# Kernel tuning notes

Measured on AMD Instinct MI355X. Metric: run time of the kernel, lower is better.

The kernel has to match this reference:

```python
import jax, jax.numpy as jnp
import numpy as np

L2_REG = 0.02


def setup_inputs() -> dict:
    key = jax.random.key(0)
    k1, k2 = jax.random.split(key)
    n, d = 4096, 1024
    anchors = jax.random.normal(k1, (n, d), dtype=jnp.float32)
    positives = jax.random.normal(k2, (n, d), dtype=jnp.float32)
    return {"anchors": anchors, "positives": positives}


def reference(anchors, positives):
    # Fused equivalent of the per-row masked_select loop:
    # x[i, j] = a_i . (p_j - p_i) = S[i, j] - S[i, i], for j != i
    n = anchors.shape[0]
    S = anchors @ positives.T                     # (n, n)
    x = S - jnp.diag(S)[:, None]                  # subtract anchor-positive sim per row
    offdiag = ~jnp.eye(n, dtype=bool)
    # sum over negatives j != i of exp(x[i, j])
    s = jnp.sum(jnp.where(offdiag, jnp.exp(x), 0.0), axis=1)  # (n,)
    n_pair = jnp.mean(jnp.log1p(s))
    l2 = jnp.sum(anchors ** 2 + positives ** 2) / n
    return n_pair + L2_REG * l2
```

## Files before the change

### kernel.cpp

```cpp
#include <hip/hip_runtime.h>
#include <math.h>
#include <stdint.h>

#define N 4096
#define Dm 1024
#define BM 128
#define BN 128
#define BK 32
#define NCB (N / 64)

typedef __attribute__((ext_vector_type(8))) short bf16x8;
typedef __attribute__((ext_vector_type(4))) float f32x4;

typedef const void __attribute__((address_space(1)))* gas_t;
typedef void __attribute__((address_space(3)))* las_t;

static __device__ __forceinline__ void gload_lds16(const void* g, void* l) {
    __builtin_amdgcn_global_load_lds((gas_t)g, (las_t)l, 16, 0, 0);
}

static __device__ __forceinline__ unsigned short f2bf(float f) {
    unsigned int u = __float_as_uint(f);
    unsigned int r = (u + 0x7fff + ((u >> 16) & 1)) >> 16;
    return (unsigned short)r;
}

__global__ __launch_bounds__(256) void prep_kernel(const float* __restrict__ A,
                                                   const float* __restrict__ P,
                                                   unsigned short* __restrict__ Abf,
                                                   unsigned short* __restrict__ Pbf,
                                                   float* __restrict__ D,
                                                   float* __restrict__ rowl2) {
    int row = blockIdx.x;
    int t = threadIdx.x;
    const float4* a4 = (const float4*)(A + (size_t)row * Dm);
    const float4* p4 = (const float4*)(P + (size_t)row * Dm);
    float4 a = a4[t], p = p4[t];
    ushort4 ab, pb;
    ab.x = f2bf(a.x); ab.y = f2bf(a.y); ab.z = f2bf(a.z); ab.w = f2bf(a.w);
    pb.x = f2bf(p.x); pb.y = f2bf(p.y); pb.z = f2bf(p.z); pb.w = f2bf(p.w);
    ((ushort4*)(Abf + (size_t)row * Dm))[t] = ab;
    ((ushort4*)(Pbf + (size_t)row * Dm))[t] = pb;
    float dot = a.x * p.x + a.y * p.y + a.z * p.z + a.w * p.w;
    float l2  = a.x * a.x + a.y * a.y + a.z * a.z + a.w * a.w
              + p.x * p.x + p.y * p.y + p.z * p.z + p.w * p.w;
#pragma unroll
    for (int off = 32; off; off >>= 1) {
        dot += __shfl_xor(dot, off, 64);
        l2  += __shfl_xor(l2,  off, 64);
    }
    __shared__ float sd[4], sl[4];
    int wave = t >> 6;
    if ((t & 63) == 0) { sd[wave] = dot; sl[wave] = l2; }
    __syncthreads();
    if (t == 0) {
        D[row]     = sd[0] + sd[1] + sd[2] + sd[3];
        rowl2[row] = sl[0] + sl[1] + sl[2] + sl[3];
    }
}

__global__ __launch_bounds__(256) void npair_mfma(const unsigned short* __restrict__ Abf,
                                                  const unsigned short* __restrict__ Pbf,
                                                  const float* __restrict__ D,
                                                  float* __restrict__ Mpart,
                                                  float* __restrict__ Spart) {
    __shared__ unsigned short At[BM * BK];
    __shared__ unsigned short Bt[BN * BK];
    int tid = threadIdx.x;
    int wid = tid >> 6, lane = tid & 63;
    int wr = wid >> 1, wc = wid & 1;
    int row0 = blockIdx.y * BM, col0 = blockIdx.x * BN;

    int r0 = tid >> 2,        kq0 = (tid & 3) << 3;
    int r1 = (256 + tid) >> 2, kq1 = (tid & 3) << 3;
    const unsigned short* Ag0 = Abf + (size_t)(row0 + r0) * Dm + kq0;
    const unsigned short* Ag1 = Abf + (size_t)(row0 + r1) * Dm + kq1;
    const unsigned short* Bg0 = Pbf + (size_t)(col0 + r0) * Dm + kq0;
    const unsigned short* Bg1 = Pbf + (size_t)(col0 + r1) * Dm + kq1;
    unsigned short* Al0 = At + (size_t)tid * 8;
    unsigned short* Al1 = At + (size_t)(256 + tid) * 8;
    unsigned short* Bl0 = Bt + (size_t)tid * 8;
    unsigned short* Bl1 = Bt + (size_t)(256 + tid) * 8;

    f32x4 acc[4][4] = {};

    for (int kt = 0; kt < Dm; kt += BK) {
        __syncthreads();
        gload_lds16(Ag0 + kt, Al0);
        gload_lds16(Ag1 + kt, Al1);
        gload_lds16(Bg0 + kt, Bl0);
        gload_lds16(Bg1 + kt, Bl1);
        __syncthreads();

        bf16x8 af[4], bfr[4];
#pragma unroll
        for (int i = 0; i < 4; ++i) {
            int arow = wr * 64 + i * 16 + (lane & 15);
            af[i]  = *(const bf16x8*)(At + arow * BK + ((lane >> 4) << 3));
            int brow = wc * 64 + i * 16 + (lane & 15);
            bfr[i] = *(const bf16x8*)(Bt + brow * BK + ((lane >> 4) << 3));
        }
#pragma unroll
        for (int i = 0; i < 4; ++i)
#pragma unroll
            for (int j = 0; j < 4; ++j)
                acc[i][j] = __builtin_amdgcn_mfma_f32_16x16x32_bf16(af[i], bfr[j], acc[i][j], 0, 0, 0);
    }

    int cb = blockIdx.x * 2 + wc;
#pragma unroll
    for (int rt = 0; rt < 4; ++rt) {
        int rbase = row0 + wr * 64 + rt * 16 + ((lane >> 4) << 2);
#pragma unroll
        for (int e = 0; e < 4; ++e) {
            int gr = rbase + e;
            float Dv = D[gr];
            float xs[4];
            float m = -INFINITY;
#pragma unroll
            for (int ct = 0; ct < 4; ++ct) {
                int gc = col0 + wc * 64 + ct * 16 + (lane & 15);
                float x = acc[rt][ct][e] - Dv;
                if (gr == gc) x = -INFINITY;
                xs[ct] = x;
                m = fmaxf(m, x);
            }
#pragma unroll
            for (int off = 8; off; off >>= 1) m = fmaxf(m, __shfl_xor(m, off, 64));
            float s = 0.0f;
#pragma unroll
            for (int ct = 0; ct < 4; ++ct) s += __expf(xs[ct] - m);
#pragma unroll
            for (int off = 8; off; off >>= 1) s += __shfl_xor(s, off, 64);
            if ((lane & 15) == 0) {
                Mpart[(size_t)gr * NCB + cb] = m;
                Spart[(size_t)gr * NCB + cb] = s;
            }
        }
    }
}

__global__ __launch_bounds__(256) void combine_rows(const float* __restrict__ Mpart,
                                                    const float* __restrict__ Spart,
                                                    float* __restrict__ loss) {
    int t = threadIdx.x;
    int lane = t & 63;
    int row = blockIdx.x * 4 + (t >> 6);
    float mp = Mpart[(size_t)row * NCB + lane];
    float sp = Spart[(size_t)row * NCB + lane];
    float m = mp;
#pragma unroll
    for (int off = 32; off; off >>= 1) m = fmaxf(m, __shfl_xor(m, off, 64));
    float s = sp * __expf(mp - m);
#pragma unroll
    for (int off = 32; off; off >>= 1) s += __shfl_xor(s, off, 64);
    if (lane == 0) loss[row] = m + logf(__expf(-m) + s);
}

__global__ __launch_bounds__(256) void final_reduce(const float* __restrict__ loss,
                                                    const float* __restrict__ rowl2,
                                                    float* __restrict__ out) {
    int t = threadIdx.x;
    float accL = 0.0f, acc2 = 0.0f;
    for (int i = t; i < N; i += 256) {
        accL += loss[i];
        acc2 += rowl2[i];
    }
#pragma unroll
    for (int off = 32; off; off >>= 1) {
        accL += __shfl_xor(accL, off, 64);
        acc2 += __shfl_xor(acc2, off, 64);
    }
    __shared__ float sa[4], sb[4];
    int wave = t >> 6;
    if ((t & 63) == 0) { sa[wave] = accL; sb[wave] = acc2; }
    __syncthreads();
    if (t == 0) {
        float L  = sa[0] + sa[1] + sa[2] + sa[3];
        float l2 = sb[0] + sb[1] + sb[2] + sb[3];
        out[0] = L / (float)N + 0.02f * (l2 / (float)N);
    }
}

extern "C" void kernel_launch(void* const* d_in, const int* in_sizes, int n_in,
                              void* d_out, int out_size, void* d_ws, size_t ws_size,
                              hipStream_t stream) {
    const float* A = (const float*)d_in[0];
    const float* P = (const float*)d_in[1];
    float* out = (float*)d_out;

    unsigned short* Abf = (unsigned short*)d_ws;
    unsigned short* Pbf = Abf + (size_t)N * Dm;
    float* D     = (float*)(Pbf + (size_t)N * Dm);
    float* rowl2 = D + N;
    float* loss  = rowl2 + N;
    float* Mpart = loss + N;
    float* Spart = Mpart + (size_t)N * NCB;

    prep_kernel<<<N, 256, 0, stream>>>(A, P, Abf, Pbf, D, rowl2);
    dim3 grid(N / BN, N / BM);
    npair_mfma<<<grid, 256, 0, stream>>>(Abf, Pbf, D, Mpart, Spart);
    combine_rows<<<N / 4, 256, 0, stream>>>(Mpart, Spart, loss);
    final_reduce<<<1, 256, 0, stream>>>(loss, rowl2, out);
}
```

Measured before the change: 141.6 us.

## Double K tile to 64 with XOR-swizzled LDS layout and cache D in shared memory

Raises the K tile from 32 to 64, so the main loop runs half as many iterations and the load/barrier overhead per MFMA is halved. The global-to-LDS copy now places 16-byte chunks under an XOR swizzle keyed on row, and the fragment reads apply the same swizzle to avoid LDS bank conflicts. The diagonal values D for the block's rows are staged in shared memory for the epilogue. LDS use doubles to 32KB, which may lower occupancy.

Result: faster. 132.1 us (-6.7%).

```diff
diff --git a/kernel.cpp b/kernel.cpp
--- a/kernel.cpp
+++ b/kernel.cpp
@@ -6,7 +6,7 @@
 #define Dm 1024
 #define BM 128
 #define BN 128
-#define BK 32
+#define BK 64
 #define NCB (N / 64)
 
 typedef __attribute__((ext_vector_type(8))) short bf16x8;
@@ -66,55 +66,63 @@
                                                   float* __restrict__ Spart) {
     __shared__ unsigned short At[BM * BK];
     __shared__ unsigned short Bt[BN * BK];
+    __shared__ float Ds[BM];
     int tid = threadIdx.x;
     int wid = tid >> 6, lane = tid & 63;
     int wr = wid >> 1, wc = wid & 1;
     int row0 = blockIdx.y * BM, col0 = blockIdx.x * BN;
 
-    int r0 = tid >> 2,        kq0 = (tid & 3) << 3;
-    int r1 = (256 + tid) >> 2, kq1 = (tid & 3) << 3;
-    const unsigned short* Ag0 = Abf + (size_t)(row0 + r0) * Dm + kq0;
-    const unsigned short* Ag1 = Abf + (size_t)(row0 + r1) * Dm + kq1;
-    const unsigned short* Bg0 = Pbf + (size_t)(col0 + r0) * Dm + kq0;
-    const unsigned short* Bg1 = Pbf + (size_t)(col0 + r1) * Dm + kq1;
-    unsigned short* Al0 = At + (size_t)tid * 8;
-    unsigned short* Al1 = At + (size_t)(256 + tid) * 8;
-    unsigned short* Bl0 = Bt + (size_t)tid * 8;
-    unsigned short* Bl1 = Bt + (size_t)(256 + tid) * 8;
+    const unsigned short* gA[4]; const unsigned short* gB[4];
+    unsigned short* lA[4]; unsigned short* lB[4];
+#pragma unroll
+    for (int b = 0; b < 4; ++b) {
+        int L = b * 256 + tid;
+        int row = L >> 3, c = L & 7;
+        int kch = c ^ (row & 7);
+        gA[b] = Abf + (size_t)(row0 + row) * Dm + (kch << 3);
+        gB[b] = Pbf + (size_t)(col0 + row) * Dm + (kch << 3);
+        lA[b] = At + (size_t)L * 8;
+        lB[b] = Bt + (size_t)L * 8;
+    }
+    if (tid < BM) Ds[tid] = D[row0 + tid];
 
     f32x4 acc[4][4] = {};
 
     for (int kt = 0; kt < Dm; kt += BK) {
         __syncthreads();
-        gload_lds16(Ag0 + kt, Al0);
-        gload_lds16(Ag1 + kt, Al1);
-        gload_lds16(Bg0 + kt, Bl0);
-        gload_lds16(Bg1 + kt, Bl1);
+#pragma unroll
+        for (int b = 0; b < 4; ++b) {
+            gload_lds16(gA[b] + kt, lA[b]);
+            gload_lds16(gB[b] + kt, lB[b]);
+        }
         __syncthreads();
-
-        bf16x8 af[4], bfr[4];
-#pragma unroll
-        for (int i = 0; i < 4; ++i) {
-            int arow = wr * 64 + i * 16 + (lane & 15);
-            af[i]  = *(const bf16x8*)(At + arow * BK + ((lane >> 4) << 3));
-            int brow = wc * 64 + i * 16 + (lane & 15);
-            bfr[i] = *(const bf16x8*)(Bt + brow * BK + ((lane >> 4) << 3));
+#pragma unroll
+        for (int ks = 0; ks < 2; ++ks) {
+            bf16x8 af[4], bfr[4];
+#pragma unroll
+            for (int i = 0; i < 4; ++i) {
+                int g = (ks << 2) + (lane >> 4);
+                int arow = wr * 64 + i * 16 + (lane & 15);
+                af[i]  = *(const bf16x8*)(At + arow * BK + ((g ^ (arow & 7)) << 3));
+                int brow = wc * 64 + i * 16 + (lane & 15);
+                bfr[i] = *(const bf16x8*)(Bt + brow * BK + ((g ^ (brow & 7)) << 3));
+            }
+#pragma unroll
+            for (int i = 0; i < 4; ++i)
+#pragma unroll
+                for (int j = 0; j < 4; ++j)
+                    acc[i][j] = __builtin_amdgcn_mfma_f32_16x16x32_bf16(af[i], bfr[j], acc[i][j], 0, 0, 0);
         }
-#pragma unroll
-        for (int i = 0; i < 4; ++i)
-#pragma unroll
-            for (int j = 0; j < 4; ++j)
-                acc[i][j] = __builtin_amdgcn_mfma_f32_16x16x32_bf16(af[i], bfr[j], acc[i][j], 0, 0, 0);
     }
 
     int cb = blockIdx.x * 2 + wc;
 #pragma unroll
     for (int rt = 0; rt < 4; ++rt) {
-        int rbase = row0 + wr * 64 + rt * 16 + ((lane >> 4) << 2);
+        int rloc = wr * 64 + rt * 16 + ((lane >> 4) << 2);
 #pragma unroll
         for (int e = 0; e < 4; ++e) {
-            int gr = rbase + e;
-            float Dv = D[gr];
+            int gr = row0 + rloc + e;
+            float Dv = Ds[rloc + e];
             float xs[4];
             float m = -INFINITY;
 #pragma unroll
```
